# Kernel tuning notes

Measured on AMD Instinct MI355X. Metric: run time of the kernel, lower is better.

Reference implementation:

```python
import jax, jax.numpy as jnp
import numpy as np

B, CTX, EMB = 4, 1024, 64
K, HID, NH = 8, 256, 8
GADD, NADD = 2, 2
RANK = 2                      # diags expand (..., k, 2) -> rank-2 index tuples
NPTS = K * (2 ** RANK + GADD + NADD)   # 64 points per token
SIGMA_BOOST = 2.0
EPS = 1e-6


def setup_inputs() -> dict:
    key = jax.random.key(0)
    ks = jax.random.split(key, 8)
    g = lambda k, shape, s: jax.random.normal(k, shape, jnp.float32) * s
    return {
        "x": g(ks[0], (B, CTX, EMB), 1.0),
        "Wq": g(ks[1], (EMB, EMB * NH), EMB ** -0.5),
        "Wk": g(ks[2], (EMB, EMB * NH), EMB ** -0.5),
        "Wv": g(ks[3], (EMB, EMB * NH), EMB ** -0.5),
        "Wu": g(ks[4], (EMB * NH, EMB), (EMB * NH) ** -0.5),
        "bu": jnp.zeros((EMB,), jnp.float32),
        "Wp1": g(ks[5], (EMB, HID), EMB ** -0.5),
        "bp1": jnp.zeros((HID,), jnp.float32),
        "Wp2": g(ks[6], (HID, 2 * K), HID ** -0.5),
        "bp2": jnp.zeros((2 * K,), jnp.float32),
        "mvalues": jnp.ones((CTX,), jnp.float32),
    }


def _forward(x, Wq, Wk, Wv, Wu, bu, Wp1, bp1, Wp2, bp2, mvalues):
    b, n, e = x.shape
    # ---- hyper network: per-token Gaussian mixture params ----
    h = jax.nn.relu(x @ Wp1 + bp1)
    params = h @ Wp2 + bp2                              # (b,n,2k)
    raw_means = params[:, :, :K][..., None]             # (b,n,k,1)
    raw_sigmas = params[:, :, K:]                       # (b,n,k)
    diags = jnp.arange(n, dtype=x.dtype)[None, :, None, None]
    means = jnp.broadcast_to(diags - jax.nn.softplus(raw_means), (b, n, K, RANK))
    means = jnp.clip(means, 0.0, n - 1.0)               # transform_means (clamp into range)
    sigmas = (jax.nn.softplus(raw_sigmas + SIGMA_BOOST) + EPS)[..., None]
    sigmas = jnp.broadcast_to(sigmas, (b, n, K, RANK))  # transform_sigmas

    # ---- ngenerate: 2^rank corners + global + local integer samples ----
    skey = jax.random.key(42)
    kg, kl = jax.random.split(skey)
    fl = jnp.floor(means).astype(jnp.int32)             # (b,n,k,2)
    offs = jnp.array([[0, 0], [0, 1], [1, 0], [1, 1]], jnp.int32)
    corners = fl[:, :, :, None, :] + offs               # (b,n,k,4,2)
    glob = jax.random.randint(kg, (b, n, K, GADD, RANK), 0, n)
    loc = fl[:, :, :, None, :] - 1 + jax.random.randint(kl, (b, n, K, NADD, RANK), 0, 2)
    idx = jnp.concatenate([corners, glob, loc], axis=3)
    idx = jnp.clip(idx, 0, n - 1).reshape(b, n, NPTS, RANK)

    # ---- nduplicates: mark repeat index tuples within each token ----
    eq = (idx[:, :, :, None, :] == idx[:, :, None, :, :]).all(-1)   # (b,n,p,p)
    tri = jnp.tril(jnp.ones((NPTS, NPTS), bool), -1)
    dup = (eq & tri).any(-1)                            # (b,n,p)

    # ---- densities: unnormalized Gaussians, zero dups, normalize over points ----
    pf = idx.astype(x.dtype)
    diff = (pf[:, :, :, None, :] - means[:, :, None, :, :]) / sigmas[:, :, None, :, :]
    dens = jnp.exp(-0.5 * (diff * diff).sum(-1))        # (b,n,p,k)
    dens = jnp.where(dup[..., None], 0.0, dens)
    dens = dens / dens.sum(axis=2, keepdims=True)
    weights = (mvalues[None, :, None, None] * dens).sum(-1)        # (b,n,p)

    # ---- heads ----
    BH = b * NH
    def heads(W):
        return (x @ W).reshape(b, n, NH, e).transpose(0, 2, 1, 3).reshape(BH, n, e)
    q = heads(Wq) / e ** 0.25
    k_ = heads(Wk) / e ** 0.25
    v = heads(Wv)

    P = n * NPTS
    idxh = jnp.broadcast_to(idx[:, None], (b, NH, n, NPTS, RANK)).reshape(BH, P, RANK)
    w = jnp.broadcast_to(weights[:, None], (b, NH, n, NPTS)).reshape(BH, P)
    rows, cols = idxh[..., 0], idxh[..., 1]

    # ---- gather q/k at sampled (row,col), per-element dot ----
    sq = jnp.take_along_axis(q, rows[:, :, None], axis=1)           # (BH,P,e)
    sk = jnp.take_along_axis(k_, cols[:, :, None], axis=1)
    dot = w * (sq * sk).sum(-1)                                     # (BH,P)

    # ---- sparse log-softmax over rows (stable, segment ops) ----
    seg = (jnp.arange(BH, dtype=jnp.int32)[:, None] * n + rows).reshape(-1)
    vflat = dot.reshape(-1)
    mx = jax.ops.segment_max(vflat, seg, num_segments=BH * n)
    ex = jnp.exp(vflat - mx[seg])
    Z = jax.ops.segment_sum(ex, seg, num_segments=BH * n)
    p = jnp.exp(vflat - (mx[seg] + jnp.log(Z[seg])))                # softmax probs

    # ---- sparse batchmm: scatter p * values[col] into rows ----
    sv = jnp.take_along_axis(v, cols[:, :, None], axis=1).reshape(-1, e)
    out = jax.ops.segment_sum(sv * p[:, None], seg, num_segments=BH * n)
    out = out.reshape(b, NH, n, e).transpose(0, 2, 1, 3).reshape(b, n, NH * e)
    return out @ Wu + bu


def reference(x, Wq, Wk, Wv, Wu, bu, Wp1, bp1, Wp2, bp2, mvalues):
    return _forward(x, Wq, Wk, Wv, Wu, bu, Wp1, bp1, Wp2, bp2, mvalues)
```

## Files before the change

kernel.cpp:

```cpp
#include <hip/hip_runtime.h>
#include <hip/hip_fp16.h>
#include <cstdint>
#include <cstddef>

#define BB 4
#define NN 1024
#define EMB_ 64
#define NH_ 8
#define BH_ (BB*NH_)
#define HID_ 256
#define K_ 8
#define NPTS_ 64
#define ROWS1 4
#define QB 1024
#define CAP 256

typedef _Float16 v2h __attribute__((ext_vector_type(2)));

__host__ __device__ inline void tf2x32(uint32_t k0, uint32_t k1, uint32_t c0, uint32_t c1,
                                       uint32_t &o0, uint32_t &o1) {
  uint32_t ks2 = k0 ^ k1 ^ 0x1BD11BDAu;
  uint32_t x0 = c0 + k0, x1 = c1 + k1;
#define TFR(r) { x0 += x1; x1 = (x1 << (r)) | (x1 >> (32 - (r))); x1 ^= x0; }
  TFR(13) TFR(15) TFR(26) TFR(6)
  x0 += k1;  x1 += ks2 + 1u;
  TFR(17) TFR(29) TFR(16) TFR(24)
  x0 += ks2; x1 += k0 + 2u;
  TFR(13) TFR(15) TFR(26) TFR(6)
  x0 += k0;  x1 += k1 + 3u;
  TFR(17) TFR(29) TFR(16) TFR(24)
  x0 += k1;  x1 += ks2 + 4u;
  TFR(13) TFR(15) TFR(26) TFR(6)
  x0 += ks2; x1 += k0 + 5u;
#undef TFR
  o0 = x0; o1 = x1;
}

__device__ inline uint32_t tf_bits(uint32_t k0, uint32_t k1, uint32_t idx) {
  uint32_t a, b;
  tf2x32(k0, k1, 0u, idx, a, b);
  return a ^ b;
}

__device__ inline float softplusf(float v) {
  return fmaxf(v, 0.f) + log1pf(expf(-fabsf(v)));
}

__global__ void __launch_bounds__(256) pre_kernel(
    const float* __restrict__ x,
    const float* __restrict__ Wq, const float* __restrict__ Wk, const float* __restrict__ Wv,
    const float* __restrict__ Wp1, const float* __restrict__ bp1,
    const float* __restrict__ Wp2, const float* __restrict__ bp2,
    const float* __restrict__ mvalues,
    __half* __restrict__ q, __half* __restrict__ k, __half* __restrict__ v,
    uint32_t* __restrict__ bucket, int* __restrict__ cursor,
    uint32_t kg0, uint32_t kg1, uint32_t kl0, uint32_t kl1) {
  __shared__ float xq[ROWS1][EMB_];
  __shared__ float xs[4][EMB_];
  __shared__ float hs[4][HID_];
  __shared__ float ps[4][16];
  __shared__ float meanv[4][K_], invsig[4][K_];
  __shared__ int flv[4][K_];
  __shared__ int pk[4][NPTS_];

  if (blockIdx.x < QB) {
    const int block0 = blockIdx.x * ROWS1;
    const int t = threadIdx.x;
    xq[t >> 6][t & 63] = x[(size_t)block0 * EMB_ + t];
    __syncthreads();
    const float qkscale = 0.3535533905932738f;

    for (int half = 0; half < 2; half++) {
      const int c = half * 256 + t;
      float aq[ROWS1], ak[ROWS1], av[ROWS1];
#pragma unroll
      for (int r = 0; r < ROWS1; r++) { aq[r] = 0.f; ak[r] = 0.f; av[r] = 0.f; }
#pragma unroll 1
      for (int i4 = 0; i4 < EMB_; i4 += 4) {
        const float q0 = Wq[(i4 + 0) * 512 + c];
        const float q1 = Wq[(i4 + 1) * 512 + c];
        const float q2 = Wq[(i4 + 2) * 512 + c];
        const float q3 = Wq[(i4 + 3) * 512 + c];
        const float k0 = Wk[(i4 + 0) * 512 + c];
        const float k1 = Wk[(i4 + 1) * 512 + c];
        const float k2 = Wk[(i4 + 2) * 512 + c];
        const float k3 = Wk[(i4 + 3) * 512 + c];
        const float v0 = Wv[(i4 + 0) * 512 + c];
        const float v1 = Wv[(i4 + 1) * 512 + c];
        const float v2 = Wv[(i4 + 2) * 512 + c];
        const float v3 = Wv[(i4 + 3) * 512 + c];
#pragma unroll
        for (int r = 0; r < ROWS1; r++) {
          const float4 xv = *(const float4*)&xq[r][i4];
          aq[r] += xv.x * q0 + xv.y * q1 + xv.z * q2 + xv.w * q3;
          ak[r] += xv.x * k0 + xv.y * k1 + xv.z * k2 + xv.w * k3;
          av[r] += xv.x * v0 + xv.y * v1 + xv.z * v2 + xv.w * v3;
        }
      }
      const int h = c >> 6, j = c & 63;
#pragma unroll
      for (int r = 0; r < ROWS1; r++) {
        const int gr = block0 + r;
        const int b = gr >> 10, n = gr & 1023;
        const size_t o = ((size_t)(b * NH_ + h) * NN + n) * EMB_ + j;
        q[o] = __float2half(aq[r] * qkscale);
        k[o] = __float2half(ak[r] * qkscale);
        v[o] = __float2half(av[r]);
      }
    }
    return;
  }

  const int w = threadIdx.x >> 6, lane = threadIdx.x & 63;
  const int bn = (blockIdx.x - QB) * 4 + w;
  const int b = bn >> 10, n = bn & 1023;

  xs[w][lane] = x[(size_t)bn * EMB_ + lane];
  __syncthreads();

#pragma unroll
  for (int cc = 0; cc < 4; cc++) {
    const int c = cc * 64 + lane;
    float a = bp1[c];
    for (int i = 0; i < EMB_; i++) a += xs[w][i] * Wp1[i * HID_ + c];
    hs[w][c] = fmaxf(a, 0.f);
  }
  __syncthreads();

  if (lane < 16) {
    float a = bp2[lane];
    for (int c = 0; c < HID_; c++) a += hs[w][c] * Wp2[c * 16 + lane];
    ps[w][lane] = a;
  }
  __syncthreads();

  if (lane < K_) {
    const float rm = ps[w][lane], rs = ps[w][K_ + lane];
    float mean = (float)n - softplusf(rm);
    mean = fminf(fmaxf(mean, 0.f), (float)(NN - 1));
    const float sig = softplusf(rs + 2.0f) + 1e-6f;
    meanv[w][lane] = mean;
    invsig[w][lane] = 1.f / sig;
    flv[w][lane] = (int)floorf(mean);
  }
  __syncthreads();

  const int kk = lane >> 3, j = lane & 7;
  const int fl = flv[w][kk];
  int row, col;
  if (j < 4) {
    row = fl + (j >> 1);
    col = fl + (j & 1);
  } else if (j < 6) {
    const int g = j - 4;
    const uint32_t base = ((uint32_t)(bn * K_ + kk) * 2u + (uint32_t)g) * 2u;
    row = (int)(tf_bits(kg0, kg1, base + 0u) & 1023u);
    col = (int)(tf_bits(kg0, kg1, base + 1u) & 1023u);
  } else {
    const int a = j - 6;
    const uint32_t base = ((uint32_t)(bn * K_ + kk) * 2u + (uint32_t)a) * 2u;
    row = fl - 1 + (int)(tf_bits(kl0, kl1, base + 0u) & 1u);
    col = fl - 1 + (int)(tf_bits(kl0, kl1, base + 1u) & 1u);
  }
  row = min(max(row, 0), NN - 1);
  col = min(max(col, 0), NN - 1);
  const int packed = (row << 16) | col;
  pk[w][lane] = packed;
  __syncthreads();

  bool dup = false;
  for (int p2 = 0; p2 < lane; p2++)
    if (pk[w][p2] == packed) dup = true;

  const float frow = (float)row, fcol = (float)col;
  float dens[K_];
#pragma unroll
  for (int qd = 0; qd < K_; qd++) {
    const float dx = (frow - meanv[w][qd]) * invsig[w][qd];
    const float dy = (fcol - meanv[w][qd]) * invsig[w][qd];
    dens[qd] = dup ? 0.f : expf(-0.5f * (dx * dx + dy * dy));
  }
  float wsum = 0.f;
#pragma unroll
  for (int qd = 0; qd < K_; qd++) {
    float s = dens[qd];
    for (int d = 1; d < 64; d <<= 1) s += __shfl_xor(s, d);
    wsum += dens[qd] / s;
  }
  const float wgt = mvalues[n] * wsum;

  const int seg = b * NN + row;
  const uint32_t payload = ((uint32_t)col << 16) |
                           (uint32_t)__half_as_ushort(__float2half(wgt));
  const int pos = atomicAdd(&cursor[seg], 1);
  if (pos < CAP) bucket[((size_t)seg << 8) + pos] = payload;
}

__global__ void __launch_bounds__(512, 6) attn_out_kernel(
    const __half* __restrict__ q, const __half* __restrict__ k, const __half* __restrict__ v,
    const int* __restrict__ cursor, const uint32_t* __restrict__ bucket,
    const float* __restrict__ Wu, const float* __restrict__ bu,
    float* __restrict__ out) {
  __shared__ __half qs[NH_][EMB_];
  __shared__ float ps_lds[NH_][64];
  __shared__ int   cs_lds[NH_][64];
  __shared__ float ao[NH_][EMB_];
  __shared__ float op[NH_][EMB_];

  const int xcd = blockIdx.x & 7;
  const int rank = blockIdx.x >> 3;
  const int b = xcd >> 1;
  const int row = (rank << 1) | (xcd & 1);

  const int h = threadIdx.x >> 6, lane = threadIdx.x & 63;
  const int bh = b * NH_ + h;

  const __half* __restrict__ kb = k + (size_t)bh * NN * EMB_;
  const __half* __restrict__ vb = v + (size_t)bh * NN * EMB_;
  const int seg = b * NN + row;
  const uint32_t* __restrict__ sp = bucket + ((size_t)seg << 8);

  qs[h][lane] = q[((size_t)bh * NN + row) * EMB_ + lane];
  const int len = min(cursor[seg], CAP);
  __syncthreads();

  float m = -INFINITY, Z = 0.f, acc = 0.f;

  for (int cb = 0; cb < len; cb += 64) {
    const int e = cb + lane;
    float logit = -INFINITY;
    int col = 0;
    if (e < len) {
      const uint32_t u = sp[e];
      col = (int)(u >> 16);
      const float wv = __half2float(__ushort_as_half((unsigned short)(u & 0xFFFFu)));
      const float4* __restrict__ kp4 = (const float4*)(kb + (size_t)col * EMB_);
      const float4* __restrict__ qp4 = (const float4*)qs[h];
      float dot = 0.f;
#pragma unroll
      for (int i = 0; i < 8; i++) {
        float4 kr = kp4[i];
        float4 qr = qp4[i];
        const v2h* ka = (const v2h*)&kr;
        const v2h* qa = (const v2h*)&qr;
#pragma unroll
        for (int jj = 0; jj < 4; jj++)
          dot = __builtin_amdgcn_fdot2(ka[jj], qa[jj], dot, false);
      }
      logit = wv * dot;
    }
    float cm = logit;
#pragma unroll
    for (int d = 1; d < 64; d <<= 1) cm = fmaxf(cm, __shfl_xor(cm, d));
    const float nm = fmaxf(m, cm);
    const float scale = expf(m - nm);
    const float p = expf(logit - nm);
    float zs = p;
#pragma unroll
    for (int d = 1; d < 64; d <<= 1) zs += __shfl_xor(zs, d);
    Z = Z * scale + zs;
    m = nm;

    ps_lds[h][lane] = p;
    cs_lds[h][lane] = col;

    acc *= scale;
    const int lim = len - cb;
#pragma unroll
    for (int g = 0; g < 8; g++) {
      if (g * 8 < lim) {
#pragma unroll
        for (int u8 = 0; u8 < 8; u8++) {
          const int ee = g * 8 + u8;
          acc += ps_lds[h][ee] * __half2float(vb[(size_t)cs_lds[h][ee] * EMB_ + lane]);
        }
      }
    }
  }

  ao[h][lane] = (len > 0) ? acc / Z : 0.f;
  __syncthreads();

  float s = 0.f;
  const float* __restrict__ wu_h = Wu + (size_t)(h * 64) * EMB_;
#pragma unroll
  for (int d = 0; d < 64; d++)
    s += ao[h][d] * wu_h[d * EMB_ + lane];
  op[h][lane] = s;
  __syncthreads();

  if (h == 0) {
    float t = bu[lane];
#pragma unroll
    for (int hh = 0; hh < NH_; hh++) t += op[hh][lane];
    out[(size_t)(b * NN + row) * EMB_ + lane] = t;
  }
}

extern "C" void kernel_launch(void* const* d_in, const int* in_sizes, int n_in,
                              void* d_out, int out_size, void* d_ws, size_t ws_size,
                              hipStream_t stream) {
  const float* x   = (const float*)d_in[0];
  const float* Wq  = (const float*)d_in[1];
  const float* Wk  = (const float*)d_in[2];
  const float* Wv  = (const float*)d_in[3];
  const float* Wu  = (const float*)d_in[4];
  const float* bu  = (const float*)d_in[5];
  const float* Wp1 = (const float*)d_in[6];
  const float* bp1 = (const float*)d_in[7];
  const float* Wp2 = (const float*)d_in[8];
  const float* bp2 = (const float*)d_in[9];
  const float* mv  = (const float*)d_in[10];
  float* out = (float*)d_out;

  char* ws = (char*)d_ws;
  size_t off = 0;
  auto alloc = [&](size_t bytes) -> void* {
    void* p = ws + off;
    off += (bytes + 255) & ~(size_t)255;
    return p;
  };
  const size_t QH = (size_t)BH_ * NN * EMB_ * sizeof(__half);
  __half*   q      = (__half*)  alloc(QH);
  __half*   k      = (__half*)  alloc(QH);
  __half*   v      = (__half*)  alloc(QH);
  uint32_t* bucket = (uint32_t*)alloc((size_t)BB * NN * CAP * sizeof(uint32_t));
  int*      cursor = (int*)     alloc((size_t)BB * NN * sizeof(int));
  if (off > ws_size) return;

  uint32_t kgA, kgB, klA, klB;
  tf2x32(0u, 42u, 0u, 0u, kgA, kgB);
  tf2x32(0u, 42u, 0u, 1u, klA, klB);
  uint32_t kg2A, kg2B, kl2A, kl2B;
  tf2x32(kgA, kgB, 0u, 1u, kg2A, kg2B);
  tf2x32(klA, klB, 0u, 1u, kl2A, kl2B);

  hipMemsetAsync(cursor, 0, (size_t)BB * NN * sizeof(int), stream);

  pre_kernel<<<QB + (BB * NN) / 4, 256, 0, stream>>>(
      x, Wq, Wk, Wv, Wp1, bp1, Wp2, bp2, mv, q, k, v, bucket, cursor,
      kg2A, kg2B, kl2A, kl2B);
  attn_out_kernel<<<BB * NN, 512, 0, stream>>>(q, k, v, cursor, bucket,
                                               Wu, bu, out);
}
```

Baseline: 158.0 us.

## Split attention-output blocks across head halves with atomic output accumulation

Each row's work is now split into two 256-thread blocks, one per group of four heads, instead of one 512-thread block covering all eight heads. The two partial Wu projections are combined with float atomicAdd into an output buffer that is zeroed beforehand. The aim is finer-grained blocks for better occupancy and load balance, since bucket lengths differ per row. The cost is an extra memset, double the global atomics on the output, and duplicated bucket and cursor reads per row.

Result: no change. 157.6 us (median of 2 runs) (-0.2%).

```diff
diff --git a/kernel.cpp b/kernel.cpp
--- a/kernel.cpp
+++ b/kernel.cpp
@@ -196,31 +196,33 @@
   if (pos < CAP) bucket[((size_t)seg << 8) + pos] = payload;
 }
 
-__global__ void __launch_bounds__(512, 6) attn_out_kernel(
+__global__ void __launch_bounds__(256, 8) attn_out_kernel(
     const __half* __restrict__ q, const __half* __restrict__ k, const __half* __restrict__ v,
     const int* __restrict__ cursor, const uint32_t* __restrict__ bucket,
     const float* __restrict__ Wu, const float* __restrict__ bu,
     float* __restrict__ out) {
-  __shared__ __half qs[NH_][EMB_];
-  __shared__ float ps_lds[NH_][64];
-  __shared__ int   cs_lds[NH_][64];
-  __shared__ float ao[NH_][EMB_];
-  __shared__ float op[NH_][EMB_];
+  __shared__ __half qs[4][EMB_];
+  __shared__ float ps_lds[4][64];
+  __shared__ int   cs_lds[4][64];
+  __shared__ float ao[4][EMB_];
+  __shared__ float op[4][EMB_];
 
   const int xcd = blockIdx.x & 7;
-  const int rank = blockIdx.x >> 3;
+  const int rid = blockIdx.x >> 3;
   const int b = xcd >> 1;
-  const int row = (rank << 1) | (xcd & 1);
-
-  const int h = threadIdx.x >> 6, lane = threadIdx.x & 63;
-  const int bh = b * NH_ + h;
+  const int row = ((rid >> 1) << 1) | (xcd & 1);
+  const int half = rid & 1;
+
+  const int hl = threadIdx.x >> 6, lane = threadIdx.x & 63;
+  const int head = half * 4 + hl;
+  const int bh = b * NH_ + head;
 
   const __half* __restrict__ kb = k + (size_t)bh * NN * EMB_;
   const __half* __restrict__ vb = v + (size_t)bh * NN * EMB_;
   const int seg = b * NN + row;
   const uint32_t* __restrict__ sp = bucket + ((size_t)seg << 8);
 
-  qs[h][lane] = q[((size_t)bh * NN + row) * EMB_ + lane];
+  qs[hl][lane] = q[((size_t)bh * NN + row) * EMB_ + lane];
   const int len = min(cursor[seg], CAP);
   __syncthreads();
 
@@ -235,7 +237,7 @@
       col = (int)(u >> 16);
       const float wv = __half2float(__ushort_as_half((unsigned short)(u & 0xFFFFu)));
       const float4* __restrict__ kp4 = (const float4*)(kb + (size_t)col * EMB_);
-      const float4* __restrict__ qp4 = (const float4*)qs[h];
+      const float4* __restrict__ qp4 = (const float4*)qs[hl];
       float dot = 0.f;
 #pragma unroll
       for (int i = 0; i < 8; i++) {
@@ -261,8 +263,8 @@
     Z = Z * scale + zs;
     m = nm;
 
-    ps_lds[h][lane] = p;
-    cs_lds[h][lane] = col;
+    ps_lds[hl][lane] = p;
+    cs_lds[hl][lane] = col;
 
     acc *= scale;
     const int lim = len - cb;
@@ -272,28 +274,28 @@
 #pragma unroll
         for (int u8 = 0; u8 < 8; u8++) {
           const int ee = g * 8 + u8;
-          acc += ps_lds[h][ee] * __half2float(vb[(size_t)cs_lds[h][ee] * EMB_ + lane]);
+          acc += ps_lds[hl][ee] * __half2float(vb[(size_t)cs_lds[hl][ee] * EMB_ + lane]);
         }
       }
     }
   }
 
-  ao[h][lane] = (len > 0) ? acc / Z : 0.f;
+  ao[hl][lane] = (len > 0) ? acc / Z : 0.f;
   __syncthreads();
 
   float s = 0.f;
-  const float* __restrict__ wu_h = Wu + (size_t)(h * 64) * EMB_;
+  const float* __restrict__ wu_h = Wu + (size_t)(head * 64) * EMB_;
 #pragma unroll
   for (int d = 0; d < 64; d++)
-    s += ao[h][d] * wu_h[d * EMB_ + lane];
-  op[h][lane] = s;
-  __syncthreads();
-
-  if (h == 0) {
-    float t = bu[lane];
-#pragma unroll
-    for (int hh = 0; hh < NH_; hh++) t += op[hh][lane];
-    out[(size_t)(b * NN + row) * EMB_ + lane] = t;
+    s += ao[hl][d] * wu_h[d * EMB_ + lane];
+  op[hl][lane] = s;
+  __syncthreads();
+
+  if (hl == 0) {
+    float t = (half == 0) ? bu[lane] : 0.f;
+#pragma unroll
+    for (int hh = 0; hh < 4; hh++) t += op[hh][lane];
+    atomicAdd(&out[(size_t)(b * NN + row) * EMB_ + lane], t);
   }
 }
 
@@ -336,10 +338,11 @@
   tf2x32(klA, klB, 0u, 1u, kl2A, kl2B);
 
   hipMemsetAsync(cursor, 0, (size_t)BB * NN * sizeof(int), stream);
+  hipMemsetAsync(out, 0, (size_t)out_size * sizeof(float), stream);
 
   pre_kernel<<<QB + (BB * NN) / 4, 256, 0, stream>>>(
       x, Wq, Wk, Wv, Wp1, bp1, Wp2, bp2, mv, q, k, v, bucket, cursor,
       kg2A, kg2B, kl2A, kl2B);
-  attn_out_kernel<<<BB * NN, 512, 0, stream>>>(q, k, v, cursor, bucket,
-                                               Wu, bu, out);
-}
+  attn_out_kernel<<<BB * NN * 2, 256, 0, stream>>>(q, k, v, cursor, bucket,
+                                                   Wu, bu, out);
+}
```
